# Kernel tuning notes

Measured on AMD Instinct MI355X. Metric: run time of the kernel, lower is better.

## Reference

```python
import jax, jax.numpy as jnp
import numpy as np

B, T, F_IN = 32, 2000, 1024
GROUPS, NUM_VARS, VQ_DIM = 2, 320, 256
VAR_DIM = VQ_DIM // GROUPS  # 128
TAU = 2.0  # curr_temp = max_temp at step 0
EPS = 1e-7


def setup_inputs() -> dict:
    key = jax.random.key(0)
    k1, k2, k3, k4 = jax.random.split(key, 4)
    x = jax.random.normal(k1, (B, T, F_IN), jnp.float32)
    # nn.Linear: weight ~ N(0,1) per module init, bias zeros
    proj_w = jax.random.normal(k2, (GROUPS * NUM_VARS, F_IN), jnp.float32)
    proj_b = jnp.zeros((GROUPS * NUM_VARS,), jnp.float32)
    # nn.init.uniform_ on vars (leading singleton dim dropped)
    codebook = jax.random.uniform(k3, (GROUPS * NUM_VARS, VAR_DIM), jnp.float32)
    # pre-sampled standard Gumbel noise (training-path gumbel_softmax)
    u = jax.random.uniform(k4, (B * T, GROUPS * NUM_VARS), jnp.float32, 1e-6, 1.0 - 1e-6)
    gumbel = -jnp.log(-jnp.log(u))
    return {"x": x, "proj_w": proj_w, "proj_b": proj_b, "codebook": codebook, "gumbel": gumbel}


def reference(x, proj_w, proj_b, codebook, gumbel):
    bsz, tsz, fsz = x.shape
    bt = bsz * tsz
    logits = x.reshape(bt, fsz) @ proj_w.T + proj_b                 # [BT, G*V]
    lg = logits.reshape(bt, GROUPS, NUM_VARS)                       # [BT, G, V]

    # hard codes (argmax of raw logits) -> code perplexity
    k = jnp.argmax(lg, axis=-1)                                     # [BT, G]
    hard_x = jax.nn.one_hot(k, NUM_VARS, dtype=lg.dtype)            # [BT, G, V]
    hard_probs = hard_x.mean(axis=0)                                # [G, V]
    code_perplexity = jnp.exp(-jnp.sum(hard_probs * jnp.log(hard_probs + EPS), -1)).sum()

    avg_probs = jax.nn.softmax(lg, axis=-1).mean(axis=0)            # [G, V]
    prob_perplex = jnp.exp(-jnp.sum(avg_probs * jnp.log(avg_probs + EPS), -1)).sum()

    # training path: gumbel_softmax(tau, hard=True) with straight-through
    g = gumbel.reshape(bt, GROUPS, NUM_VARS)
    y_soft = jax.nn.softmax((lg + g) / TAU, axis=-1)                # [BT, G, V]
    y_hard = jax.nn.one_hot(jnp.argmax(y_soft, -1), NUM_VARS, dtype=y_soft.dtype)
    y = y_hard + y_soft - jax.lax.stop_gradient(y_soft)             # straight-through

    # codebook weighted sum; original does (one_hot[...,None] * vars).sum over V
    cb = codebook.reshape(GROUPS, NUM_VARS, VAR_DIM)
    q = jnp.einsum("tgv,gvd->tgd", y, cb)                           # [BT, G, var_dim]
    q = q.reshape(bsz, tsz, VQ_DIM)
    return q, code_perplexity, prob_perplex
```

## Files before the change

### kernel.cpp

```cpp
#include <hip/hip_runtime.h>
#include <cstdint>
#include <cstddef>

#define BT_TOT 64000
#define FIN    1024
#define GV     640
#define NV     320
#define VD     128
#define INV_BT (1.0f/64000.0f)

#define WTILE_B 40960

typedef __attribute__((ext_vector_type(8))) __bf16 bf16x8;
typedef __attribute__((ext_vector_type(16))) float f32x16;

typedef __attribute__((address_space(1))) void gvoid_t;
typedef __attribute__((address_space(3))) void lvoid_t;

__device__ inline short f2bf(float x) {
    unsigned int u = __float_as_uint(x);
    unsigned int r = (u + 0x7fffu + ((u >> 16) & 1u)) >> 16;
    return (short)r;
}
__device__ inline float bf2f(short h) {
    return __uint_as_float(((unsigned int)(unsigned short)h) << 16);
}
__device__ inline bf16x8 ld_frag(const short* p) {
    union { uint4 u; bf16x8 v; } t;
    t.u = *(const uint4*)p;
    return t.v;
}
__device__ __forceinline__ void glds16(const void* g, void* l) {
    __builtin_amdgcn_global_load_lds((gvoid_t*)g, (lvoid_t*)l, 16, 0, 0);
}

__global__ __launch_bounds__(256) void prep(
    const float* __restrict__ W, char* __restrict__ Wpk,
    float* __restrict__ psum_g, int* __restrict__ cnt_g)
{
    const int t = blockIdx.x * 256 + threadIdx.x;
    if (t < GV) { psum_g[t] = 0.f; cnt_g[t] = 0; }
    const int r   = t >> 7;
    const int ck8 = t & 127;
    const int kt  = ck8 >> 1;
    const int ch  = ck8 & 1;
    const float* src = W + (size_t)r * FIN + (size_t)ck8 * 8;
    const float4 a = ((const float4*)src)[0];
    const float4 b = ((const float4*)src)[1];
    float xs[8] = {a.x, a.y, a.z, a.w, b.x, b.y, b.z, b.w};
    short hi[8], lo[8];
#pragma unroll
    for (int e = 0; e < 8; ++e) {
        hi[e] = f2bf(xs[e]);
        lo[e] = f2bf(xs[e] - bf2f(hi[e]));
    }
    char* dst = Wpk + (size_t)kt * WTILE_B + (size_t)r * 32 + ch * 16;
    *(uint4*)dst             = *(uint4*)hi;
    *(uint4*)(dst + 20480)   = *(uint4*)lo;
}

__global__ __launch_bounds__(512, 2) void fused(
    const float* __restrict__ X, const char* __restrict__ Wpk,
    const float* __restrict__ bias, const float* __restrict__ gumbel,
    const float* __restrict__ codebook, float* __restrict__ q,
    float* __restrict__ psum_g, int* __restrict__ cnt_g)
{
    __shared__ __align__(16) char smem[2 * WTILE_B];

    const int tid  = threadIdx.x;
    const int lane = tid & 63, wave = tid >> 6;
    const int mw = wave & 3, nw = wave >> 2;
    const int cl = lane & 31, h = lane >> 5;
    const int row0 = blockIdx.x * 128;
    const int arow = mw * 32 + cl;

    f32x16 acc[10];
#pragma unroll
    for (int nt = 0; nt < 10; ++nt) acc[nt] = (f32x16)0.0f;

    const float* aptr = X + (size_t)(row0 + arow) * FIN + h * 8;

    float4 xa0, xa1;
    {
#pragma unroll
        for (int i = 0; i < 5; ++i) {
            const int task = tid + 512 * i;
            glds16(Wpk + (size_t)task * 16, smem + task * 16);
        }
        __builtin_amdgcn_sched_barrier(0);
        xa0 = *(const float4*)(aptr);
        xa1 = *(const float4*)(aptr + 4);
    }

    for (int t = 0; t < 64; ++t) {
        asm volatile("s_waitcnt vmcnt(2)" ::: "memory");
        __builtin_amdgcn_s_barrier();

        const char* bufc = smem + (t & 1) * WTILE_B;
        float4 na0, na1;
        if (t < 63) {
            char* bufn = smem + ((t + 1) & 1) * WTILE_B;
            const char* wt = Wpk + (size_t)(t + 1) * WTILE_B;
#pragma unroll
            for (int i = 0; i < 5; ++i) {
                const int task = tid + 512 * i;
                glds16(wt + (size_t)task * 16, bufn + task * 16);
            }
            __builtin_amdgcn_sched_barrier(0);
            const float* ap = aptr + (t + 1) * 16;
            na0 = *(const float4*)(ap);
            na1 = *(const float4*)(ap + 4);
        }
        __builtin_amdgcn_sched_barrier(0);

        union { float4 f[2]; float s[8]; } ua;
        ua.f[0] = xa0; ua.f[1] = xa1;
        union { short s[8]; bf16x8 v; } uh, ul;
#pragma unroll
        for (int e = 0; e < 8; ++e) {
            const short hb = f2bf(ua.s[e]);
            uh.s[e] = hb;
            ul.s[e] = f2bf(ua.s[e] - bf2f(hb));
        }
        const bf16x8 a_h = uh.v, a_l = ul.v;

        __builtin_amdgcn_s_setprio(1);
#pragma unroll
        for (int nt = 0; nt < 10; ++nt) {
            const int bcol = nw * 320 + nt * 32 + cl;
            const bf16x8 b_h = ld_frag((const short*)(bufc + bcol * 32 + h * 16));
            const bf16x8 b_l = ld_frag((const short*)(bufc + 20480 + bcol * 32 + h * 16));
            acc[nt] = __builtin_amdgcn_mfma_f32_32x32x16_bf16(a_h, b_h, acc[nt], 0, 0, 0);
            acc[nt] = __builtin_amdgcn_mfma_f32_32x32x16_bf16(a_l, b_h, acc[nt], 0, 0, 0);
            acc[nt] = __builtin_amdgcn_mfma_f32_32x32x16_bf16(a_h, b_l, acc[nt], 0, 0, 0);
        }
        __builtin_amdgcn_s_setprio(0);

        xa0 = na0; xa1 = na1;
    }

    float* psum_l = (float*)(smem);
    int*   cnt_l  = (int*)(smem + 2560);
    int*   gidx   = (int*)(smem + 5120);

    for (int i = tid; i < GV; i += 512) { psum_l[i] = 0.f; cnt_l[i] = 0; }
    __syncthreads();

#pragma unroll
    for (int nt = 0; nt < 10; ++nt) {
        const float bv = bias[nw * 320 + nt * 32 + cl];
#pragma unroll
        for (int r = 0; r < 16; ++r) acc[nt][r] += bv;
    }

    float pcol[10];
#pragma unroll
    for (int nt = 0; nt < 10; ++nt) pcol[nt] = 0.f;

#pragma unroll
    for (int reg = 0; reg < 16; ++reg) {
        const int rloc = mw * 32 + (reg & 3) + 8 * (reg >> 2) + 4 * h;
        const float* gp = gumbel + (size_t)(row0 + rloc) * GV + nw * 320;
        float bestv = -3.4e38f, gbv = -3.4e38f;
        int bestc = 0, gbc = 0;
#pragma unroll
        for (int nt = 0; nt < 10; ++nt) {
            const float v = acc[nt][reg];
            const int cc = nt * 32 + cl;
            const float tv = v + gp[cc];
            if (v > bestv) { bestv = v; bestc = cc; }
            if (tv > gbv)  { gbv = tv;  gbc = cc; }
        }
#pragma unroll
        for (int off = 1; off < 32; off <<= 1) {
            const float v2 = __shfl_xor(bestv, off); const int c2 = __shfl_xor(bestc, off);
            if (v2 > bestv || (v2 == bestv && c2 < bestc)) { bestv = v2; bestc = c2; }
            const float g2 = __shfl_xor(gbv, off); const int gc2 = __shfl_xor(gbc, off);
            if (g2 > gbv || (g2 == gbv && gc2 < gbc)) { gbv = g2; gbc = gc2; }
        }
        float e[10], s = 0.f;
#pragma unroll
        for (int nt = 0; nt < 10; ++nt) { e[nt] = __expf(acc[nt][reg] - bestv); s += e[nt]; }
#pragma unroll
        for (int off = 1; off < 32; off <<= 1) s += __shfl_xor(s, off);
        const float inv_s = 1.0f / s;
#pragma unroll
        for (int nt = 0; nt < 10; ++nt) pcol[nt] += e[nt] * inv_s;
        if (cl == 0) {
            atomicAdd(&cnt_l[nw * 320 + bestc], 1);
            gidx[rloc * 2 + nw] = nw * 320 + gbc;
        }
    }
#pragma unroll
    for (int nt = 0; nt < 10; ++nt) {
        const float v = pcol[nt] + __shfl_xor(pcol[nt], 32);
        if (h == 0) atomicAdd(&psum_l[nw * 320 + nt * 32 + cl], v);
    }
    __syncthreads();

    {
        const int unit = tid >> 1, half = tid & 1;
        const int row = unit >> 1, gq = unit & 1;
        const int idx = gidx[row * 2 + gq];
        const float4* srcp = (const float4*)(codebook + (size_t)idx * VD + half * 64);
        float4* dstp = (float4*)(q + (size_t)(row0 + row) * 256 + gq * VD + half * 64);
#pragma unroll
        for (int i = 0; i < 16; ++i) dstp[i] = srcp[i];
    }
    for (int i = tid; i < GV; i += 512) {
        atomicAdd(&psum_g[i], psum_l[i]);
        atomicAdd(&cnt_g[i], cnt_l[i]);
    }
}

__global__ void finalize(const int* __restrict__ cnt_g, const float* __restrict__ psum_g,
                         float* __restrict__ out_scalars)
{
    const int lane = threadIdx.x;
    float hsum[2] = {0.f, 0.f}, p[2] = {0.f, 0.f};
    for (int i = lane; i < GV; i += 64) {
        const int g = i / NV;
        const float hp = (float)cnt_g[i] * INV_BT;
        const float ap = psum_g[i] * INV_BT;
        hsum[g] -= hp * logf(hp + 1e-7f);
        p[g]    -= ap * logf(ap + 1e-7f);
    }
#pragma unroll
    for (int off = 32; off > 0; off >>= 1) {
        hsum[0] += __shfl_xor(hsum[0], off); hsum[1] += __shfl_xor(hsum[1], off);
        p[0] += __shfl_xor(p[0], off);       p[1] += __shfl_xor(p[1], off);
    }
    if (lane == 0) {
        out_scalars[0] = expf(hsum[0]) + expf(hsum[1]);
        out_scalars[1] = expf(p[0]) + expf(p[1]);
    }
}

extern "C" void kernel_launch(void* const* d_in, const int* in_sizes, int n_in,
                              void* d_out, int out_size, void* d_ws, size_t ws_size,
                              hipStream_t stream)
{
    const float* X  = (const float*)d_in[0];
    const float* W  = (const float*)d_in[1];
    const float* Bv = (const float*)d_in[2];
    const float* CB = (const float*)d_in[3];
    const float* GU = (const float*)d_in[4];

    float* q = (float*)d_out;
    float* out_scalars = (float*)d_out + (size_t)BT_TOT * 256;

    char* ws = (char*)d_ws;
    float* psum_g = (float*)ws;
    int*   cnt_g  = (int*)(ws + 4096);
    char*  Wpk    = ws + 8192;

    prep<<<320, 256, 0, stream>>>(W, Wpk, psum_g, cnt_g);
    fused<<<500, 512, 0, stream>>>(X, Wpk, Bv, GU, CB, q, psum_g, cnt_g);
    finalize<<<1, 64, 0, stream>>>(cnt_g, psum_g, out_scalars);
}
```

Measured before the change: 719.4 us.

## Split fused GEMM blocks by codebook group with 256-row tiles and XCD swizzle

Each block now handles one codebook group (320 columns) for 256 rows using 1024 threads, instead of all 640 columns for 128 rows with 512 threads. The packed weight layout is reordered per group, so each block streams only half the weight tile into LDS. Block IDs are remapped so that the two groups of a row block land near each other across XCDs. Because each group's columns are split across two waves, the softmax and argmax reductions now merge partial results through shared memory. This reduces LDS footprint and weight traffic per block, but X rows are now read by two blocks and extra barriers are added to the epilogue.

Measured after the change: 706.9 us. Within noise of the previous version (-1.7%).

```diff
diff --git a/kernel.cpp b/kernel.cpp
--- a/kernel.cpp
+++ b/kernel.cpp
@@ -10,6 +10,7 @@
 #define INV_BT (1.0f/64000.0f)
 
 #define WTILE_B 40960
+#define GTILE_B 20480
 
 typedef __attribute__((ext_vector_type(8))) __bf16 bf16x8;
 typedef __attribute__((ext_vector_type(16))) float f32x16;
@@ -25,7 +26,7 @@
 __device__ inline float bf2f(short h) {
     return __uint_as_float(((unsigned int)(unsigned short)h) << 16);
 }
-__device__ inline bf16x8 ld_frag(const short* p) {
+__device__ inline bf16x8 ld_frag(const char* p) {
     union { uint4 u; bf16x8 v; } t;
     t.u = *(const uint4*)p;
     return t.v;
@@ -43,7 +44,9 @@
     const int r   = t >> 7;
     const int ck8 = t & 127;
     const int kt  = ck8 >> 1;
-    const int ch  = ck8 & 1;
+    const int chk = ck8 & 1;
+    const int g   = (r >= NV) ? 1 : 0;
+    const int c   = r - g * NV;
     const float* src = W + (size_t)r * FIN + (size_t)ck8 * 8;
     const float4 a = ((const float4*)src)[0];
     const float4 b = ((const float4*)src)[1];
@@ -54,39 +57,46 @@
         hi[e] = f2bf(xs[e]);
         lo[e] = f2bf(xs[e] - bf2f(hi[e]));
     }
-    char* dst = Wpk + (size_t)kt * WTILE_B + (size_t)r * 32 + ch * 16;
-    *(uint4*)dst             = *(uint4*)hi;
-    *(uint4*)(dst + 20480)   = *(uint4*)lo;
-}
-
-__global__ __launch_bounds__(512, 2) void fused(
+    const int u = c * 2 + chk;
+    char* base = Wpk + (size_t)kt * WTILE_B + (size_t)g * GTILE_B;
+    *(uint4*)(base + u * 16)         = *(uint4*)hi;
+    *(uint4*)(base + 10240 + u * 16) = *(uint4*)lo;
+}
+
+__global__ __launch_bounds__(1024, 4) void fused(
     const float* __restrict__ X, const char* __restrict__ Wpk,
     const float* __restrict__ bias, const float* __restrict__ gumbel,
     const float* __restrict__ codebook, float* __restrict__ q,
     float* __restrict__ psum_g, int* __restrict__ cnt_g)
 {
-    __shared__ __align__(16) char smem[2 * WTILE_B];
+    __shared__ __align__(16) char smem[2 * GTILE_B];
+
+    const int id = blockIdx.x;
+    const int linear = (id & 7) * 64 + (id >> 3);
+    if (linear >= 500) return;
+    const int rb = linear >> 1, g = linear & 1;
 
     const int tid  = threadIdx.x;
     const int lane = tid & 63, wave = tid >> 6;
-    const int mw = wave & 3, nw = wave >> 2;
+    const int stripe = wave >> 1, ch = wave & 1;
     const int cl = lane & 31, h = lane >> 5;
-    const int row0 = blockIdx.x * 128;
-    const int arow = mw * 32 + cl;
-
-    f32x16 acc[10];
-#pragma unroll
-    for (int nt = 0; nt < 10; ++nt) acc[nt] = (f32x16)0.0f;
+    const int row0 = rb * 256;
+    const int arow = stripe * 32 + cl;
+
+    const int u2 = 1024 + (tid & 255);
+    const int rdbase = ch * 5120 + cl * 32 + h * 16;
+
+    f32x16 acc[5];
+#pragma unroll
+    for (int nt = 0; nt < 5; ++nt) acc[nt] = (f32x16)0.0f;
 
     const float* aptr = X + (size_t)(row0 + arow) * FIN + h * 8;
+    const char*  wbase = Wpk + (size_t)g * GTILE_B;
 
     float4 xa0, xa1;
     {
-#pragma unroll
-        for (int i = 0; i < 5; ++i) {
-            const int task = tid + 512 * i;
-            glds16(Wpk + (size_t)task * 16, smem + task * 16);
-        }
+        glds16(wbase + (size_t)tid * 16, smem + tid * 16);
+        glds16(wbase + (size_t)u2 * 16,  smem + u2 * 16);
         __builtin_amdgcn_sched_barrier(0);
         xa0 = *(const float4*)(aptr);
         xa1 = *(const float4*)(aptr + 4);
@@ -95,21 +105,14 @@
     for (int t = 0; t < 64; ++t) {
         asm volatile("s_waitcnt vmcnt(2)" ::: "memory");
         __builtin_amdgcn_s_barrier();
-
-        const char* bufc = smem + (t & 1) * WTILE_B;
-        float4 na0, na1;
+        __builtin_amdgcn_sched_barrier(0);
+
+        const char* bufc = smem + (t & 1) * GTILE_B;
         if (t < 63) {
-            char* bufn = smem + ((t + 1) & 1) * WTILE_B;
-            const char* wt = Wpk + (size_t)(t + 1) * WTILE_B;
-#pragma unroll
-            for (int i = 0; i < 5; ++i) {
-                const int task = tid + 512 * i;
-                glds16(wt + (size_t)task * 16, bufn + task * 16);
-            }
-            __builtin_amdgcn_sched_barrier(0);
-            const float* ap = aptr + (t + 1) * 16;
-            na0 = *(const float4*)(ap);
-            na1 = *(const float4*)(ap + 4);
+            char* bufn = smem + ((t + 1) & 1) * GTILE_B;
+            const char* wt = wbase + (size_t)(t + 1) * WTILE_B;
+            glds16(wt + (size_t)tid * 16, bufn + tid * 16);
+            glds16(wt + (size_t)u2 * 16,  bufn + u2 * 16);
         }
         __builtin_amdgcn_sched_barrier(0);
 
@@ -123,93 +126,130 @@
             ul.s[e] = f2bf(ua.s[e] - bf2f(hb));
         }
         const bf16x8 a_h = uh.v, a_l = ul.v;
+        __builtin_amdgcn_sched_barrier(0);
+
+        if (t < 63) {
+            const float* ap = aptr + (t + 1) * 16;
+            xa0 = *(const float4*)(ap);
+            xa1 = *(const float4*)(ap + 4);
+        }
+        __builtin_amdgcn_sched_barrier(0);
 
         __builtin_amdgcn_s_setprio(1);
 #pragma unroll
-        for (int nt = 0; nt < 10; ++nt) {
-            const int bcol = nw * 320 + nt * 32 + cl;
-            const bf16x8 b_h = ld_frag((const short*)(bufc + bcol * 32 + h * 16));
-            const bf16x8 b_l = ld_frag((const short*)(bufc + 20480 + bcol * 32 + h * 16));
+        for (int nt = 0; nt < 5; ++nt) {
+            const bf16x8 b_h = ld_frag(bufc + nt * 1024 + rdbase);
+            const bf16x8 b_l = ld_frag(bufc + 10240 + nt * 1024 + rdbase);
             acc[nt] = __builtin_amdgcn_mfma_f32_32x32x16_bf16(a_h, b_h, acc[nt], 0, 0, 0);
             acc[nt] = __builtin_amdgcn_mfma_f32_32x32x16_bf16(a_l, b_h, acc[nt], 0, 0, 0);
             acc[nt] = __builtin_amdgcn_mfma_f32_32x32x16_bf16(a_h, b_l, acc[nt], 0, 0, 0);
         }
         __builtin_amdgcn_s_setprio(0);
-
-        xa0 = na0; xa1 = na1;
     }
 
     float* psum_l = (float*)(smem);
-    int*   cnt_l  = (int*)(smem + 2560);
-    int*   gidx   = (int*)(smem + 5120);
-
-    for (int i = tid; i < GV; i += 512) { psum_l[i] = 0.f; cnt_l[i] = 0; }
+    int*   cnt_l  = (int*)(smem + 1280);
+    int*   gidx   = (int*)(smem + 2560);
+    float* sv  = (float*)(smem + 4096);
+    int*   sc  = (int*)(smem + 6144);
+    float* sgv = (float*)(smem + 8192);
+    int*   sgc = (int*)(smem + 10240);
+    float* ss  = (float*)(smem + 12288);
+
+    for (int i = tid; i < NV; i += 1024) { psum_l[i] = 0.f; cnt_l[i] = 0; }
+
+#pragma unroll
+    for (int nt = 0; nt < 5; ++nt) {
+        const float bv = bias[g * NV + ch * 160 + nt * 32 + cl];
+#pragma unroll
+        for (int r = 0; r < 16; ++r) acc[nt][r] += bv;
+    }
+
+    float pcol[5];
+#pragma unroll
+    for (int nt = 0; nt < 5; ++nt) pcol[nt] = 0.f;
+
+#pragma unroll
+    for (int c0 = 0; c0 < 16; c0 += 4) {
+        float bv[4], gv[4], sl[4];
+        int bc[4], gc[4];
+#pragma unroll
+        for (int j = 0; j < 4; ++j) {
+            const int reg = c0 + j;
+            const int rloc = stripe * 32 + (reg & 3) + 8 * (reg >> 2) + 4 * h;
+            const float* gp = gumbel + (size_t)(row0 + rloc) * GV + g * NV;
+            float bestv = -3.4e38f, gbv = -3.4e38f;
+            int bestc = 0, gbc = 0;
+#pragma unroll
+            for (int nt = 0; nt < 5; ++nt) {
+                const float v = acc[nt][reg];
+                const int cc = ch * 160 + nt * 32 + cl;
+                const float tv = v + gp[cc];
+                if (v > bestv) { bestv = v; bestc = cc; }
+                if (tv > gbv)  { gbv = tv;  gbc = cc; }
+            }
+#pragma unroll
+            for (int off = 1; off < 32; off <<= 1) {
+                const float v2 = __shfl_xor(bestv, off); const int c2 = __shfl_xor(bestc, off);
+                if (v2 > bestv || (v2 == bestv && c2 < bestc)) { bestv = v2; bestc = c2; }
+                const float g2 = __shfl_xor(gbv, off); const int gc2 = __shfl_xor(gbc, off);
+                if (g2 > gbv || (g2 == gbv && gc2 < gbc)) { gbv = g2; gbc = gc2; }
+            }
+            float s = 0.f;
+#pragma unroll
+            for (int nt = 0; nt < 5; ++nt) s += __expf(acc[nt][reg] - bestv);
+#pragma unroll
+            for (int off = 1; off < 32; off <<= 1) s += __shfl_xor(s, off);
+            bv[j] = bestv; bc[j] = bestc; gv[j] = gbv; gc[j] = gbc; sl[j] = s;
+            if (cl == 0) {
+                const int si = rloc * 2 + ch;
+                sv[si] = bestv; sc[si] = bestc; sgv[si] = gbv; sgc[si] = gbc; ss[si] = s;
+            }
+        }
+        __syncthreads();
+#pragma unroll
+        for (int j = 0; j < 4; ++j) {
+            const int reg = c0 + j;
+            const int rloc = stripe * 32 + (reg & 3) + 8 * (reg >> 2) + 4 * h;
+            const int pi = rloc * 2 + (ch ^ 1);
+            const float pv = sv[pi]; const int pc = sc[pi];
+            const float pgv = sgv[pi]; const int pgc = sgc[pi];
+            const float ps = ss[pi];
+            float m = bv[j]; int mc = bc[j];
+            if (pv > m || (pv == m && pc < mc)) { m = pv; mc = pc; }
+            float mg = gv[j]; int mgc = gc[j];
+            if (pgv > mg || (pgv == mg && pgc < mgc)) { mg = pgv; mgc = pgc; }
+            const float fl = __expf(bv[j] - m);
+            const float stot = sl[j] * fl + ps * __expf(pv - m);
+            const float fscale = fl / stot;
+#pragma unroll
+            for (int nt = 0; nt < 5; ++nt)
+                pcol[nt] += __expf(acc[nt][reg] - bv[j]) * fscale;
+            if (ch == 0 && cl == 0) {
+                atomicAdd(&cnt_l[mc], 1);
+                gidx[rloc] = mgc;
+            }
+        }
+    }
+
+#pragma unroll
+    for (int nt = 0; nt < 5; ++nt) {
+        const float v = pcol[nt] + __shfl_xor(pcol[nt], 32);
+        if (h == 0) atomicAdd(&psum_l[ch * 160 + nt * 32 + cl], v);
+    }
     __syncthreads();
 
-#pragma unroll
-    for (int nt = 0; nt < 10; ++nt) {
-        const float bv = bias[nw * 320 + nt * 32 + cl];
-#pragma unroll
-        for (int r = 0; r < 16; ++r) acc[nt][r] += bv;
-    }
-
-    float pcol[10];
-#pragma unroll
-    for (int nt = 0; nt < 10; ++nt) pcol[nt] = 0.f;
-
-#pragma unroll
-    for (int reg = 0; reg < 16; ++reg) {
-        const int rloc = mw * 32 + (reg & 3) + 8 * (reg >> 2) + 4 * h;
-        const float* gp = gumbel + (size_t)(row0 + rloc) * GV + nw * 320;
-        float bestv = -3.4e38f, gbv = -3.4e38f;
-        int bestc = 0, gbc = 0;
-#pragma unroll
-        for (int nt = 0; nt < 10; ++nt) {
-            const float v = acc[nt][reg];
-            const int cc = nt * 32 + cl;
-            const float tv = v + gp[cc];
-            if (v > bestv) { bestv = v; bestc = cc; }
-            if (tv > gbv)  { gbv = tv;  gbc = cc; }
-        }
-#pragma unroll
-        for (int off = 1; off < 32; off <<= 1) {
-            const float v2 = __shfl_xor(bestv, off); const int c2 = __shfl_xor(bestc, off);
-            if (v2 > bestv || (v2 == bestv && c2 < bestc)) { bestv = v2; bestc = c2; }
-            const float g2 = __shfl_xor(gbv, off); const int gc2 = __shfl_xor(gbc, off);
-            if (g2 > gbv || (g2 == gbv && gc2 < gbc)) { gbv = g2; gbc = gc2; }
-        }
-        float e[10], s = 0.f;
-#pragma unroll
-        for (int nt = 0; nt < 10; ++nt) { e[nt] = __expf(acc[nt][reg] - bestv); s += e[nt]; }
-#pragma unroll
-        for (int off = 1; off < 32; off <<= 1) s += __shfl_xor(s, off);
-        const float inv_s = 1.0f / s;
-#pragma unroll
-        for (int nt = 0; nt < 10; ++nt) pcol[nt] += e[nt] * inv_s;
-        if (cl == 0) {
-            atomicAdd(&cnt_l[nw * 320 + bestc], 1);
-            gidx[rloc * 2 + nw] = nw * 320 + gbc;
-        }
-    }
-#pragma unroll
-    for (int nt = 0; nt < 10; ++nt) {
-        const float v = pcol[nt] + __shfl_xor(pcol[nt], 32);
-        if (h == 0) atomicAdd(&psum_l[nw * 320 + nt * 32 + cl], v);
-    }
-    __syncthreads();
-
     {
-        const int unit = tid >> 1, half = tid & 1;
-        const int row = unit >> 1, gq = unit & 1;
-        const int idx = gidx[row * 2 + gq];
-        const float4* srcp = (const float4*)(codebook + (size_t)idx * VD + half * 64);
-        float4* dstp = (float4*)(q + (size_t)(row0 + row) * 256 + gq * VD + half * 64);
-#pragma unroll
-        for (int i = 0; i < 16; ++i) dstp[i] = srcp[i];
-    }
-    for (int i = tid; i < GV; i += 512) {
-        atomicAdd(&psum_g[i], psum_l[i]);
-        atomicAdd(&cnt_g[i], cnt_l[i]);
+        const int row = tid >> 2, quarter = tid & 3;
+        const int idx = g * NV + gidx[row];
+        const float4* srcp = (const float4*)(codebook + (size_t)idx * VD + quarter * 32);
+        float4* dstp = (float4*)(q + (size_t)(row0 + row) * 256 + g * VD + quarter * 32);
+#pragma unroll
+        for (int i = 0; i < 8; ++i) dstp[i] = srcp[i];
+    }
+    for (int i = tid; i < NV; i += 1024) {
+        atomicAdd(&psum_g[g * NV + i], psum_l[i]);
+        atomicAdd(&cnt_g[g * NV + i], cnt_l[i]);
     }
 }
 
@@ -255,6 +295,6 @@
     char*  Wpk    = ws + 8192;
 
     prep<<<320, 256, 0, stream>>>(W, Wpk, psum_g, cnt_g);
-    fused<<<500, 512, 0, stream>>>(X, Wpk, Bv, GU, CB, q, psum_g, cnt_g);
+    fused<<<512, 1024, 0, stream>>>(X, Wpk, Bv, GU, CB, q, psum_g, cnt_g);
     finalize<<<1, 64, 0, stream>>>(cnt_g, psum_g, out_scalars);
 }
```

## Retile fused GEMM to 256-row x one-group blocks with deeper K steps

Applied to the files above, without the earlier changes.

Each block now covers 256 rows and one codebook group (320 columns) instead of 128 rows and both groups, and processes K in 32-wide steps split into four sub-phases with interleaved LDS fragment loads and global prefetch. The W pack layout is reordered per group and iteration to match. Block IDs are swizzled across 512 launched blocks (12 exit early) so that the two group blocks sharing an X tile land together, and the occupancy hint of 2 blocks per SM is dropped. The aim is to raise MFMA work per LDS byte and overlap loads better. The cost is that each X row is now read by two blocks, and the extra barriers per iteration may add stalls.

Result: faster. 664.1 us (-7.7%).

```diff
diff --git a/kernel.cpp b/kernel.cpp
--- a/kernel.cpp
+++ b/kernel.cpp
@@ -9,7 +9,8 @@
 #define VD     128
 #define INV_BT (1.0f/64000.0f)
 
-#define WTILE_B 40960
+#define ITER_B  81920
+#define BUF_B   40960
 
 typedef __attribute__((ext_vector_type(8))) __bf16 bf16x8;
 typedef __attribute__((ext_vector_type(16))) float f32x16;
@@ -25,13 +26,25 @@
 __device__ inline float bf2f(short h) {
     return __uint_as_float(((unsigned int)(unsigned short)h) << 16);
 }
-__device__ inline bf16x8 ld_frag(const short* p) {
+__device__ inline bf16x8 ld_frag(const char* p) {
     union { uint4 u; bf16x8 v; } t;
     t.u = *(const uint4*)p;
     return t.v;
 }
 __device__ __forceinline__ void glds16(const void* g, void* l) {
     __builtin_amdgcn_global_load_lds((gvoid_t*)g, (lvoid_t*)l, 16, 0, 0);
+}
+__device__ __forceinline__ void cvt8(const float4 f0, const float4 f1,
+                                     bf16x8& hh, bf16x8& ll) {
+    union { float4 f[2]; float s[8]; } ua; ua.f[0] = f0; ua.f[1] = f1;
+    union { short s[8]; bf16x8 v; } uh, ul;
+#pragma unroll
+    for (int e = 0; e < 8; ++e) {
+        const short hb = f2bf(ua.s[e]);
+        uh.s[e] = hb;
+        ul.s[e] = f2bf(ua.s[e] - bf2f(hb));
+    }
+    hh = uh.v; ll = ul.v;
 }
 
 __global__ __launch_bounds__(256) void prep(
@@ -40,10 +53,13 @@
 {
     const int t = blockIdx.x * 256 + threadIdx.x;
     if (t < GV) { psum_g[t] = 0.f; cnt_g[t] = 0; }
-    const int r   = t >> 7;
-    const int ck8 = t & 127;
-    const int kt  = ck8 >> 1;
-    const int ch  = ck8 & 1;
+    const int r    = t >> 7;
+    const int ck8  = t & 127;
+    const int iter = ck8 >> 2;
+    const int c    = (ck8 >> 1) & 1;
+    const int ch   = ck8 & 1;
+    const int g    = (r >= NV) ? 1 : 0;
+    const int cv   = r - g * NV;
     const float* src = W + (size_t)r * FIN + (size_t)ck8 * 8;
     const float4 a = ((const float4*)src)[0];
     const float4 b = ((const float4*)src)[1];
@@ -54,101 +70,169 @@
         hi[e] = f2bf(xs[e]);
         lo[e] = f2bf(xs[e] - bf2f(hi[e]));
     }
-    char* dst = Wpk + (size_t)kt * WTILE_B + (size_t)r * 32 + ch * 16;
-    *(uint4*)dst             = *(uint4*)hi;
-    *(uint4*)(dst + 20480)   = *(uint4*)lo;
-}
-
-__global__ __launch_bounds__(512, 2) void fused(
+    char* dst = Wpk + (size_t)iter * ITER_B + (size_t)g * BUF_B + (size_t)c * 20480
+                    + (size_t)(cv * 32 + ch * 16);
+    *(uint4*)dst           = *(uint4*)hi;
+    *(uint4*)(dst + 10240) = *(uint4*)lo;
+}
+
+__global__ __launch_bounds__(512) void fused(
     const float* __restrict__ X, const char* __restrict__ Wpk,
     const float* __restrict__ bias, const float* __restrict__ gumbel,
     const float* __restrict__ codebook, float* __restrict__ q,
     float* __restrict__ psum_g, int* __restrict__ cnt_g)
 {
-    __shared__ __align__(16) char smem[2 * WTILE_B];
+    __shared__ __align__(16) char smem[2 * BUF_B];
+
+    const int id = blockIdx.x;
+    const int linear = (id & 7) * 64 + (id >> 3);
+    if (linear >= 500) return;
+    const int rb = linear >> 1, g = linear & 1;
 
     const int tid  = threadIdx.x;
     const int lane = tid & 63, wave = tid >> 6;
-    const int mw = wave & 3, nw = wave >> 2;
     const int cl = lane & 31, h = lane >> 5;
-    const int row0 = blockIdx.x * 128;
-    const int arow = mw * 32 + cl;
+    const int row0 = rb * 256;
+    const int arow = wave * 32 + cl;
+    const int rdo  = cl * 32 + h * 16;
 
     f32x16 acc[10];
 #pragma unroll
     for (int nt = 0; nt < 10; ++nt) acc[nt] = (f32x16)0.0f;
 
-    const float* aptr = X + (size_t)(row0 + arow) * FIN + h * 8;
-
-    float4 xa0, xa1;
+    const float* aptr  = X + (size_t)(row0 + arow) * FIN + h * 8;
+    const char*  wbase = Wpk + (size_t)g * BUF_B;
+
+    float4 xa0, xa1, xa2, xa3;
     {
 #pragma unroll
-        for (int i = 0; i < 5; ++i) {
-            const int task = tid + 512 * i;
-            glds16(Wpk + (size_t)task * 16, smem + task * 16);
-        }
+        for (int j = 0; j < 5; ++j)
+            glds16(wbase + (size_t)(tid + 512 * j) * 16, smem + (tid + 512 * j) * 16);
         __builtin_amdgcn_sched_barrier(0);
         xa0 = *(const float4*)(aptr);
         xa1 = *(const float4*)(aptr + 4);
-    }
-
-    for (int t = 0; t < 64; ++t) {
+        xa2 = *(const float4*)(aptr + 16);
+        xa3 = *(const float4*)(aptr + 20);
+        asm volatile("s_waitcnt vmcnt(4)" ::: "memory");
+        __builtin_amdgcn_s_barrier();
+    }
+
+    for (int i = 0; i < 32; ++i) {
+        const char* bufc = smem + (i & 1) * BUF_B;
+        char* bufn = smem + ((i + 1) & 1) * BUF_B;
+        const char* wsrc = wbase + (size_t)(i + 1) * ITER_B;
+        const float* apn = aptr + (i + 1) * 32;
+        const bool more = (i < 31);
+        bf16x8 bh[5], bl[5], ah, al;
+
+#pragma unroll
+        for (int n = 0; n < 5; ++n) {
+            bh[n] = ld_frag(bufc + n * 1024 + rdo);
+            bl[n] = ld_frag(bufc + 10240 + n * 1024 + rdo);
+        }
+        if (more) {
+            glds16(wsrc + (size_t)tid * 16,         bufn + tid * 16);
+            glds16(wsrc + (size_t)(tid + 512) * 16, bufn + (tid + 512) * 16);
+        }
+        cvt8(xa0, xa1, ah, al);
+        __builtin_amdgcn_sched_barrier(0);
+        __builtin_amdgcn_s_barrier();
+        asm volatile("s_waitcnt lgkmcnt(0)" ::: "memory");
+        __builtin_amdgcn_sched_barrier(0);
+        __builtin_amdgcn_s_setprio(1);
+#pragma unroll
+        for (int n = 0; n < 5; ++n) {
+            acc[n] = __builtin_amdgcn_mfma_f32_32x32x16_bf16(ah, bh[n], acc[n], 0, 0, 0);
+            acc[n] = __builtin_amdgcn_mfma_f32_32x32x16_bf16(al, bh[n], acc[n], 0, 0, 0);
+            acc[n] = __builtin_amdgcn_mfma_f32_32x32x16_bf16(ah, bl[n], acc[n], 0, 0, 0);
+        }
+        __builtin_amdgcn_s_setprio(0);
+        __builtin_amdgcn_s_barrier();
+
+#pragma unroll
+        for (int n = 0; n < 5; ++n) {
+            bh[n] = ld_frag(bufc + (n + 5) * 1024 + rdo);
+            bl[n] = ld_frag(bufc + 10240 + (n + 5) * 1024 + rdo);
+        }
+        if (more)
+            glds16(wsrc + (size_t)(tid + 1024) * 16, bufn + (tid + 1024) * 16);
+        __builtin_amdgcn_sched_barrier(0);
+        __builtin_amdgcn_s_barrier();
+        asm volatile("s_waitcnt lgkmcnt(0)" ::: "memory");
+        __builtin_amdgcn_sched_barrier(0);
+        __builtin_amdgcn_s_setprio(1);
+#pragma unroll
+        for (int n = 0; n < 5; ++n) {
+            acc[n + 5] = __builtin_amdgcn_mfma_f32_32x32x16_bf16(ah, bh[n], acc[n + 5], 0, 0, 0);
+            acc[n + 5] = __builtin_amdgcn_mfma_f32_32x32x16_bf16(al, bh[n], acc[n + 5], 0, 0, 0);
+            acc[n + 5] = __builtin_amdgcn_mfma_f32_32x32x16_bf16(ah, bl[n], acc[n + 5], 0, 0, 0);
+        }
+        __builtin_amdgcn_s_setprio(0);
+        __builtin_amdgcn_s_barrier();
+
+#pragma unroll
+        for (int n = 0; n < 5; ++n) {
+            bh[n] = ld_frag(bufc + 20480 + n * 1024 + rdo);
+            bl[n] = ld_frag(bufc + 30720 + n * 1024 + rdo);
+        }
+        if (more) {
+            glds16(wsrc + (size_t)(tid + 1536) * 16, bufn + (tid + 1536) * 16);
+            __builtin_amdgcn_sched_barrier(0);
+            xa0 = *(const float4*)(apn);
+            xa1 = *(const float4*)(apn + 4);
+        }
+        cvt8(xa2, xa3, ah, al);
+        __builtin_amdgcn_sched_barrier(0);
+        __builtin_amdgcn_s_barrier();
+        asm volatile("s_waitcnt lgkmcnt(0)" ::: "memory");
+        __builtin_amdgcn_sched_barrier(0);
+        __builtin_amdgcn_s_setprio(1);
+#pragma unroll
+        for (int n = 0; n < 5; ++n) {
+            acc[n] = __builtin_amdgcn_mfma_f32_32x32x16_bf16(ah, bh[n], acc[n], 0, 0, 0);
+            acc[n] = __builtin_amdgcn_mfma_f32_32x32x16_bf16(al, bh[n], acc[n], 0, 0, 0);
+            acc[n] = __builtin_amdgcn_mfma_f32_32x32x16_bf16(ah, bl[n], acc[n], 0, 0, 0);
+        }
+        __builtin_amdgcn_s_setprio(0);
+        __builtin_amdgcn_s_barrier();
+
+#pragma unroll
+        for (int n = 0; n < 5; ++n) {
+            bh[n] = ld_frag(bufc + 20480 + (n + 5) * 1024 + rdo);
+            bl[n] = ld_frag(bufc + 30720 + (n + 5) * 1024 + rdo);
+        }
+        if (more) {
+            glds16(wsrc + (size_t)(tid + 2048) * 16, bufn + (tid + 2048) * 16);
+            __builtin_amdgcn_sched_barrier(0);
+            xa2 = *(const float4*)(apn + 16);
+            xa3 = *(const float4*)(apn + 20);
+        }
+        __builtin_amdgcn_sched_barrier(0);
+        __builtin_amdgcn_s_barrier();
+        asm volatile("s_waitcnt lgkmcnt(0)" ::: "memory");
+        __builtin_amdgcn_sched_barrier(0);
+        __builtin_amdgcn_s_setprio(1);
+#pragma unroll
+        for (int n = 0; n < 5; ++n) {
+            acc[n + 5] = __builtin_amdgcn_mfma_f32_32x32x16_bf16(ah, bh[n], acc[n + 5], 0, 0, 0);
+            acc[n + 5] = __builtin_amdgcn_mfma_f32_32x32x16_bf16(al, bh[n], acc[n + 5], 0, 0, 0);
+            acc[n + 5] = __builtin_amdgcn_mfma_f32_32x32x16_bf16(ah, bl[n], acc[n + 5], 0, 0, 0);
+        }
+        __builtin_amdgcn_s_setprio(0);
         asm volatile("s_waitcnt vmcnt(2)" ::: "memory");
         __builtin_amdgcn_s_barrier();
-
-        const char* bufc = smem + (t & 1) * WTILE_B;
-        float4 na0, na1;
-        if (t < 63) {
-            char* bufn = smem + ((t + 1) & 1) * WTILE_B;
-            const char* wt = Wpk + (size_t)(t + 1) * WTILE_B;
-#pragma unroll
-            for (int i = 0; i < 5; ++i) {
-                const int task = tid + 512 * i;
-                glds16(wt + (size_t)task * 16, bufn + task * 16);
-            }
-            __builtin_amdgcn_sched_barrier(0);
-            const float* ap = aptr + (t + 1) * 16;
-            na0 = *(const float4*)(ap);
-            na1 = *(const float4*)(ap + 4);
-        }
-        __builtin_amdgcn_sched_barrier(0);
-
-        union { float4 f[2]; float s[8]; } ua;
-        ua.f[0] = xa0; ua.f[1] = xa1;
-        union { short s[8]; bf16x8 v; } uh, ul;
-#pragma unroll
-        for (int e = 0; e < 8; ++e) {
-            const short hb = f2bf(ua.s[e]);
-            uh.s[e] = hb;
-            ul.s[e] = f2bf(ua.s[e] - bf2f(hb));
-        }
-        const bf16x8 a_h = uh.v, a_l = ul.v;
-
-        __builtin_amdgcn_s_setprio(1);
-#pragma unroll
-        for (int nt = 0; nt < 10; ++nt) {
-            const int bcol = nw * 320 + nt * 32 + cl;
-            const bf16x8 b_h = ld_frag((const short*)(bufc + bcol * 32 + h * 16));
-            const bf16x8 b_l = ld_frag((const short*)(bufc + 20480 + bcol * 32 + h * 16));
-            acc[nt] = __builtin_amdgcn_mfma_f32_32x32x16_bf16(a_h, b_h, acc[nt], 0, 0, 0);
-            acc[nt] = __builtin_amdgcn_mfma_f32_32x32x16_bf16(a_l, b_h, acc[nt], 0, 0, 0);
-            acc[nt] = __builtin_amdgcn_mfma_f32_32x32x16_bf16(a_h, b_l, acc[nt], 0, 0, 0);
-        }
-        __builtin_amdgcn_s_setprio(0);
-
-        xa0 = na0; xa1 = na1;
     }
 
     float* psum_l = (float*)(smem);
-    int*   cnt_l  = (int*)(smem + 2560);
-    int*   gidx   = (int*)(smem + 5120);
-
-    for (int i = tid; i < GV; i += 512) { psum_l[i] = 0.f; cnt_l[i] = 0; }
+    int*   cnt_l  = (int*)(smem + 1280);
+    int*   gidx   = (int*)(smem + 2560);
+
+    for (int i = tid; i < NV; i += 512) { psum_l[i] = 0.f; cnt_l[i] = 0; }
     __syncthreads();
 
 #pragma unroll
     for (int nt = 0; nt < 10; ++nt) {
-        const float bv = bias[nw * 320 + nt * 32 + cl];
+        const float bv = bias[g * NV + nt * 32 + cl];
 #pragma unroll
         for (int r = 0; r < 16; ++r) acc[nt][r] += bv;
     }
@@ -159,8 +243,8 @@
 
 #pragma unroll
     for (int reg = 0; reg < 16; ++reg) {
-        const int rloc = mw * 32 + (reg & 3) + 8 * (reg >> 2) + 4 * h;
-        const float* gp = gumbel + (size_t)(row0 + rloc) * GV + nw * 320;
+        const int rloc = wave * 32 + (reg & 3) + 8 * (reg >> 2) + 4 * h;
+        const float* gp = gumbel + (size_t)(row0 + rloc) * GV + g * NV;
         float bestv = -3.4e38f, gbv = -3.4e38f;
         int bestc = 0, gbc = 0;
 #pragma unroll
@@ -187,29 +271,28 @@
 #pragma unroll
         for (int nt = 0; nt < 10; ++nt) pcol[nt] += e[nt] * inv_s;
         if (cl == 0) {
-            atomicAdd(&cnt_l[nw * 320 + bestc], 1);
-            gidx[rloc * 2 + nw] = nw * 320 + gbc;
+            atomicAdd(&cnt_l[bestc], 1);
+            gidx[rloc] = gbc;
         }
     }
 #pragma unroll
     for (int nt = 0; nt < 10; ++nt) {
         const float v = pcol[nt] + __shfl_xor(pcol[nt], 32);
-        if (h == 0) atomicAdd(&psum_l[nw * 320 + nt * 32 + cl], v);
+        if (h == 0) atomicAdd(&psum_l[nt * 32 + cl], v);
     }
     __syncthreads();
 
     {
-        const int unit = tid >> 1, half = tid & 1;
-        const int row = unit >> 1, gq = unit & 1;
-        const int idx = gidx[row * 2 + gq];
+        const int row = tid >> 1, half = tid & 1;
+        const int idx = g * NV + gidx[row];
         const float4* srcp = (const float4*)(codebook + (size_t)idx * VD + half * 64);
-        float4* dstp = (float4*)(q + (size_t)(row0 + row) * 256 + gq * VD + half * 64);
+        float4* dstp = (float4*)(q + (size_t)(row0 + row) * 256 + g * VD + half * 64);
 #pragma unroll
         for (int i = 0; i < 16; ++i) dstp[i] = srcp[i];
     }
-    for (int i = tid; i < GV; i += 512) {
-        atomicAdd(&psum_g[i], psum_l[i]);
-        atomicAdd(&cnt_g[i], cnt_l[i]);
+    for (int i = tid; i < NV; i += 512) {
+        atomicAdd(&psum_g[g * NV + i], psum_l[i]);
+        atomicAdd(&cnt_g[g * NV + i], cnt_l[i]);
     }
 }
 
@@ -255,6 +338,6 @@
     char*  Wpk    = ws + 8192;
 
     prep<<<320, 256, 0, stream>>>(W, Wpk, psum_g, cnt_g);
-    fused<<<500, 512, 0, stream>>>(X, Wpk, Bv, GU, CB, q, psum_g, cnt_g);
+    fused<<<512, 512, 0, stream>>>(X, Wpk, Bv, GU, CB, q, psum_g, cnt_g);
     finalize<<<1, 64, 0, stream>>>(cnt_g, psum_g, out_scalars);
 }
```
